# Kernel tuning notes

Measured on AMD Instinct MI355X. Metric: run time of the kernel, lower is better.

## Reference

```python
import jax, jax.numpy as jnp
import numpy as np
import math

NEG = -1000000.0

def setup_inputs() -> dict:
    key = jax.random.key(0)
    k1, k2, k3, k4 = jax.random.split(key, 4)
    B, S, D = 64, 1024, 64
    query = jax.random.normal(k1, (B, S, D), dtype=jnp.float32)
    key_t = jax.random.normal(k2, (B, S, D), dtype=jnp.float32)
    value = jax.random.normal(k3, (B, S, D), dtype=jnp.float32)
    valid_lens = jax.random.randint(k4, (B,), 1, S + 1, dtype=jnp.int32)
    return {"query": query, "key": key_t, "value": value, "valid_lens": valid_lens}

def reference(query, key, value, valid_lens):
    # query/key/value: [B, S, D]; valid_lens: [B]
    d = query.shape[-1]
    scores = jnp.einsum('bqd,bkd->bqk', query, key) / math.sqrt(d)
    Sk = key.shape[1]
    # 1D valid_lens -> same mask for every query row (repeat_interleave semantics)
    mask = jnp.arange(Sk)[None, None, :] < valid_lens[:, None, None]  # [B,1,Sk]
    scores = jnp.where(mask, scores, NEG)
    weights = jax.nn.softmax(scores, axis=-1)
    # dropout p=0.0 -> identity
    return jnp.einsum('bqk,bkd->bqd', weights, value)
```

## Files before the change

kernel.cpp:

```cpp
#include <hip/hip_runtime.h>
#include <hip/hip_bf16.h>
#include <cstdint>


typedef __attribute__((ext_vector_type(8))) short short8;
typedef __attribute__((ext_vector_type(4))) float f32x4;

#define B_   64
#define S_   1024
#define D_   64
#define BQ   64
#define BK   64
#define KPAD 72

__device__ __forceinline__ uint32_t pk2(float a, float b) {
    float2 t; t.x = a; t.y = b;
    union { __hip_bfloat162 h; uint32_t u; } c;
    c.h = __float22bfloat162_rn(t);
    return c.u;
}

__global__ __launch_bounds__(256, 4)
void attn_fwd(const float* __restrict__ Q, const float* __restrict__ K,
              const float* __restrict__ V, const int* __restrict__ VL,
              float* __restrict__ Out) {
    __shared__ __align__(16) unsigned short lK [BK * KPAD];
    __shared__ __align__(16) unsigned short lVt[D_ * 64];
    __shared__ __align__(16) unsigned short lP [4 * 16 * KPAD];

    const int tid  = threadIdx.x;
    const int wave = tid >> 6;
    const int lane = tid & 63;
    const int col  = lane & 15;
    const int quad = lane >> 4;

    const int bid  = blockIdx.x;
    const int b    = (bid & 7) * 8 + (bid >> 7);
    const int q0   = ((bid >> 3) & 15) * BQ;
    const int vlen = VL[b];
    const int ntiles = (vlen + BK - 1) / BK;

    const int T  = tid >> 4;
    const int m  = tid & 15;
    const int Tl = T & 3;
    const int cb = T >> 2;
    const int dcs = m >> 1;
    const int sws = ((dcs & 1) << 2) | (dcs >> 1);

    const float* Kb = K + (size_t)b * S_ * D_ + 4 * m;
    const float* Vb = V + (size_t)b * S_ * D_ + 4 * m;

    float4 kr[4], vr[4];
    #pragma unroll
    for (int j = 0; j < 4; ++j) {
        const int row = 2 * T + (j >> 1) * 32 + (j & 1);
        kr[j] = *(const float4*)(Kb + (size_t)row * D_);
        vr[j] = *(const float4*)(Vb + (size_t)row * D_);
    }

    short8 qa[2];
    {
        const int qrow = q0 + wave * 16 + col;
        const float* qp = Q + ((size_t)b * S_ + qrow) * D_ + quad * 8;
        #pragma unroll
        for (int c = 0; c < 2; ++c) {
            float4 x0 = *(const float4*)(qp + c * 32);
            float4 x1 = *(const float4*)(qp + c * 32 + 4);
            union { uint32_t u[4]; short8 s; } qq;
            qq.u[0] = pk2(x0.x, x0.y);
            qq.u[1] = pk2(x0.z, x0.w);
            qq.u[2] = pk2(x1.x, x1.y);
            qq.u[3] = pk2(x1.z, x1.w);
            qa[c] = qq.s;
        }
    }

    f32x4 ofrag[4];
    #pragma unroll
    for (int dt = 0; dt < 4; ++dt) ofrag[dt] = (f32x4){0.f, 0.f, 0.f, 0.f};
    float lsum = 0.f;

    const float cexp = 0.18033688011112042f;
    unsigned short* pw = &lP[wave * 16 * KPAD];

    for (int kt = 0; kt < ntiles; ++kt) {
        const int kbase = kt * BK;

        __syncthreads();

        #pragma unroll
        for (int j = 0; j < 4; ++j) {
            const int row = 2 * T + (j >> 1) * 32 + (j & 1);
            uint2 kv;
            kv.x = pk2(kr[j].x, kr[j].y);
            kv.y = pk2(kr[j].z, kr[j].w);
            *(uint2*)&lK[row * KPAD + 4 * m] = kv;
        }
        #pragma unroll
        for (int i = 0; i < 2; ++i) {
            const int p = (cb + 4 * i) ^ sws;
            unsigned short* base = &lVt[p * 8 + 2 * Tl];
            const float4 va = vr[2 * i], vb2 = vr[2 * i + 1];
            *(uint32_t*)&base[(4 * m + 0) * 64] = pk2(va.x, vb2.x);
            *(uint32_t*)&base[(4 * m + 1) * 64] = pk2(va.y, vb2.y);
            *(uint32_t*)&base[(4 * m + 2) * 64] = pk2(va.z, vb2.z);
            *(uint32_t*)&base[(4 * m + 3) * 64] = pk2(va.w, vb2.w);
        }

        if (kt + 1 < ntiles) {
            const size_t off = (size_t)(kt + 1) * BK * D_;
            #pragma unroll
            for (int j = 0; j < 4; ++j) {
                const int row = 2 * T + (j >> 1) * 32 + (j & 1);
                kr[j] = *(const float4*)(Kb + off + (size_t)row * D_);
                vr[j] = *(const float4*)(Vb + off + (size_t)row * D_);
            }
        }

        __syncthreads();

        f32x4 sfrag[4];
        #pragma unroll
        for (int ct = 0; ct < 4; ++ct) {
            f32x4 acc = (f32x4){0.f, 0.f, 0.f, 0.f};
            #pragma unroll
            for (int c = 0; c < 2; ++c) {
                short8 kf = *(const short8*)&lK[(ct * 16 + col) * KPAD + c * 32 + quad * 8];
                acc = __builtin_amdgcn_mfma_f32_16x16x32_bf16(kf, qa[c], acc, 0, 0, 0);
            }
            sfrag[ct] = acc;
        }

        if (kbase + BK <= vlen) {
            #pragma unroll
            for (int ct = 0; ct < 4; ++ct) {
                float e0 = __builtin_amdgcn_exp2f(sfrag[ct][0] * cexp);
                float e1 = __builtin_amdgcn_exp2f(sfrag[ct][1] * cexp);
                float e2 = __builtin_amdgcn_exp2f(sfrag[ct][2] * cexp);
                float e3 = __builtin_amdgcn_exp2f(sfrag[ct][3] * cexp);
                lsum += (e0 + e1) + (e2 + e3);
                uint2 pk; pk.x = pk2(e0, e1); pk.y = pk2(e2, e3);
                *(uint2*)&pw[col * KPAD + ct * 16 + quad * 4] = pk;
            }
        } else {
            #pragma unroll
            for (int ct = 0; ct < 4; ++ct) {
                const int kv0 = kbase + ct * 16 + quad * 4;
                float e[4];
                #pragma unroll
                for (int rr = 0; rr < 4; ++rr) {
                    e[rr] = (kv0 + rr < vlen)
                          ? __builtin_amdgcn_exp2f(sfrag[ct][rr] * cexp) : 0.0f;
                    lsum += e[rr];
                }
                uint2 pk; pk.x = pk2(e[0], e[1]); pk.y = pk2(e[2], e[3]);
                *(uint2*)&pw[col * KPAD + ct * 16 + quad * 4] = pk;
            }
        }

        #pragma unroll
        for (int kc = 0; kc < 2; ++kc) {
            short8 pa = *(const short8*)&pw[col * KPAD + kc * 32 + quad * 8];
            #pragma unroll
            for (int dt = 0; dt < 4; ++dt) {
                const int sr = ((col >> 3) << 2) | dt;
                const int p  = (kc * 4 + quad) ^ sr;
                short8 vb = *(const short8*)&lVt[(dt * 16 + col) * 64 + p * 8];
                ofrag[dt] = __builtin_amdgcn_mfma_f32_16x16x32_bf16(pa, vb, ofrag[dt], 0, 0, 0);
            }
        }
    }

    float s = lsum;
    s += __shfl_xor(s, 16, 64);
    s += __shfl_xor(s, 32, 64);
    const int qrow0 = q0 + wave * 16 + quad * 4;
    #pragma unroll
    for (int rr = 0; rr < 4; ++rr) {
        const float inv = 1.0f / __shfl(s, quad * 4 + rr, 64);
        float* op = Out + ((size_t)b * S_ + qrow0 + rr) * D_ + col;
        #pragma unroll
        for (int dt = 0; dt < 4; ++dt)
            op[dt * 16] = ofrag[dt][rr] * inv;
    }
}

extern "C" void kernel_launch(void* const* d_in, const int* in_sizes, int n_in,
                              void* d_out, int out_size, void* d_ws, size_t ws_size,
                              hipStream_t stream) {
    const float* Q  = (const float*)d_in[0];
    const float* K  = (const float*)d_in[1];
    const float* V  = (const float*)d_in[2];
    const int*   VL = (const int*)d_in[3];
    float* Out = (float*)d_out;
    dim3 grid(B_ * (S_ / BQ));
    attn_fwd<<<grid, 256, 0, stream>>>(Q, K, V, VL, Out);
}
```

Baseline: 115.0 us.

## Load K fragments directly from global per wave and double-buffer V in LDS

K is no longer staged through shared memory. Each wave loads its K MFMA fragments straight from global memory and converts them to bf16 in registers. V staging becomes double-buffered, which cuts the loop to one barrier per tile. This removes the K LDS writes and reads and one __syncthreads per iteration. In exchange, each of the four waves in a block now reads the whole K tile from global or L2 (4x redundant) with no prefetch, so load latency may be exposed. An unused pbf helper is also added.

After: 188.9 us. 1.64x slower.

```diff
diff --git a/kernel.cpp b/kernel.cpp
--- a/kernel.cpp
+++ b/kernel.cpp
@@ -11,7 +11,7 @@
 #define D_   64
 #define BQ   64
 #define BK   64
-#define KPAD 72
+#define PPAD 72
 
 __device__ __forceinline__ uint32_t pk2(float a, float b) {
     float2 t; t.x = a; t.y = b;
@@ -19,14 +19,17 @@
     c.h = __float22bfloat162_rn(t);
     return c.u;
 }
+__device__ __forceinline__ unsigned short pbf(float f) {
+    union { float f; uint32_t u; } v; v.f = f;
+    return (unsigned short)((v.u + 0x8000u) >> 16);
+}
 
 __global__ __launch_bounds__(256, 4)
 void attn_fwd(const float* __restrict__ Q, const float* __restrict__ K,
               const float* __restrict__ V, const int* __restrict__ VL,
               float* __restrict__ Out) {
-    __shared__ __align__(16) unsigned short lK [BK * KPAD];
-    __shared__ __align__(16) unsigned short lVt[D_ * 64];
-    __shared__ __align__(16) unsigned short lP [4 * 16 * KPAD];
+    __shared__ __align__(16) unsigned short lVt[2][D_ * 64];
+    __shared__ __align__(16) unsigned short lP [4 * 16 * PPAD];
 
     const int tid  = threadIdx.x;
     const int wave = tid >> 6;
@@ -47,14 +50,12 @@
     const int dcs = m >> 1;
     const int sws = ((dcs & 1) << 2) | (dcs >> 1);
 
-    const float* Kb = K + (size_t)b * S_ * D_ + 4 * m;
     const float* Vb = V + (size_t)b * S_ * D_ + 4 * m;
 
-    float4 kr[4], vr[4];
+    float4 vr[4];
     #pragma unroll
     for (int j = 0; j < 4; ++j) {
         const int row = 2 * T + (j >> 1) * 32 + (j & 1);
-        kr[j] = *(const float4*)(Kb + (size_t)row * D_);
         vr[j] = *(const float4*)(Vb + (size_t)row * D_);
     }
 
@@ -75,31 +76,24 @@
         }
     }
 
+    const float* Kw = K + ((size_t)b * S_ + col) * D_ + quad * 8;
+
     f32x4 ofrag[4];
     #pragma unroll
     for (int dt = 0; dt < 4; ++dt) ofrag[dt] = (f32x4){0.f, 0.f, 0.f, 0.f};
     float lsum = 0.f;
 
     const float cexp = 0.18033688011112042f;
-    unsigned short* pw = &lP[wave * 16 * KPAD];
+    unsigned short* pw = &lP[wave * 16 * PPAD];
 
     for (int kt = 0; kt < ntiles; ++kt) {
         const int kbase = kt * BK;
-
-        __syncthreads();
-
-        #pragma unroll
-        for (int j = 0; j < 4; ++j) {
-            const int row = 2 * T + (j >> 1) * 32 + (j & 1);
-            uint2 kv;
-            kv.x = pk2(kr[j].x, kr[j].y);
-            kv.y = pk2(kr[j].z, kr[j].w);
-            *(uint2*)&lK[row * KPAD + 4 * m] = kv;
-        }
+        unsigned short* bV = lVt[kt & 1];
+
         #pragma unroll
         for (int i = 0; i < 2; ++i) {
             const int p = (cb + 4 * i) ^ sws;
-            unsigned short* base = &lVt[p * 8 + 2 * Tl];
+            unsigned short* base = &bV[p * 8 + 2 * Tl];
             const float4 va = vr[2 * i], vb2 = vr[2 * i + 1];
             *(uint32_t*)&base[(4 * m + 0) * 64] = pk2(va.x, vb2.x);
             *(uint32_t*)&base[(4 * m + 1) * 64] = pk2(va.y, vb2.y);
@@ -107,40 +101,51 @@
             *(uint32_t*)&base[(4 * m + 3) * 64] = pk2(va.w, vb2.w);
         }
 
+        __syncthreads();
+
         if (kt + 1 < ntiles) {
-            const size_t off = (size_t)(kt + 1) * BK * D_;
+            const float* vp = Vb + (size_t)(kbase + BK) * D_;
             #pragma unroll
             for (int j = 0; j < 4; ++j) {
                 const int row = 2 * T + (j >> 1) * 32 + (j & 1);
-                kr[j] = *(const float4*)(Kb + off + (size_t)row * D_);
-                vr[j] = *(const float4*)(Vb + off + (size_t)row * D_);
-            }
-        }
-
-        __syncthreads();
-
-        f32x4 sfrag[4];
-        #pragma unroll
-        for (int ct = 0; ct < 4; ++ct) {
-            f32x4 acc = (f32x4){0.f, 0.f, 0.f, 0.f};
-            #pragma unroll
-            for (int c = 0; c < 2; ++c) {
-                short8 kf = *(const short8*)&lK[(ct * 16 + col) * KPAD + c * 32 + quad * 8];
-                acc = __builtin_amdgcn_mfma_f32_16x16x32_bf16(kf, qa[c], acc, 0, 0, 0);
-            }
-            sfrag[ct] = acc;
+                vr[j] = *(const float4*)(vp + (size_t)row * D_);
+            }
+        }
+
+        f32x4 sf[4];
+        #pragma unroll
+        for (int ct = 0; ct < 4; ++ct) sf[ct] = (f32x4){0.f, 0.f, 0.f, 0.f};
+        const float* Kt = Kw + (size_t)kbase * D_;
+        #pragma unroll
+        for (int c = 0; c < 2; ++c) {
+            short8 kf[4];
+            #pragma unroll
+            for (int ct = 0; ct < 4; ++ct) {
+                const float* kp = Kt + ct * 16 * D_ + c * 32;
+                float4 x0 = *(const float4*)kp;
+                float4 x1 = *(const float4*)(kp + 4);
+                union { uint32_t u[4]; short8 s; } kk;
+                kk.u[0] = pk2(x0.x, x0.y);
+                kk.u[1] = pk2(x0.z, x0.w);
+                kk.u[2] = pk2(x1.x, x1.y);
+                kk.u[3] = pk2(x1.z, x1.w);
+                kf[ct] = kk.s;
+            }
+            #pragma unroll
+            for (int ct = 0; ct < 4; ++ct)
+                sf[ct] = __builtin_amdgcn_mfma_f32_16x16x32_bf16(kf[ct], qa[c], sf[ct], 0, 0, 0);
         }
 
         if (kbase + BK <= vlen) {
             #pragma unroll
             for (int ct = 0; ct < 4; ++ct) {
-                float e0 = __builtin_amdgcn_exp2f(sfrag[ct][0] * cexp);
-                float e1 = __builtin_amdgcn_exp2f(sfrag[ct][1] * cexp);
-                float e2 = __builtin_amdgcn_exp2f(sfrag[ct][2] * cexp);
-                float e3 = __builtin_amdgcn_exp2f(sfrag[ct][3] * cexp);
+                float e0 = __builtin_amdgcn_exp2f(sf[ct][0] * cexp);
+                float e1 = __builtin_amdgcn_exp2f(sf[ct][1] * cexp);
+                float e2 = __builtin_amdgcn_exp2f(sf[ct][2] * cexp);
+                float e3 = __builtin_amdgcn_exp2f(sf[ct][3] * cexp);
                 lsum += (e0 + e1) + (e2 + e3);
                 uint2 pk; pk.x = pk2(e0, e1); pk.y = pk2(e2, e3);
-                *(uint2*)&pw[col * KPAD + ct * 16 + quad * 4] = pk;
+                *(uint2*)&pw[col * PPAD + ct * 16 + quad * 4] = pk;
             }
         } else {
             #pragma unroll
@@ -150,22 +155,22 @@
                 #pragma unroll
                 for (int rr = 0; rr < 4; ++rr) {
                     e[rr] = (kv0 + rr < vlen)
-                          ? __builtin_amdgcn_exp2f(sfrag[ct][rr] * cexp) : 0.0f;
+                          ? __builtin_amdgcn_exp2f(sf[ct][rr] * cexp) : 0.0f;
                     lsum += e[rr];
                 }
                 uint2 pk; pk.x = pk2(e[0], e[1]); pk.y = pk2(e[2], e[3]);
-                *(uint2*)&pw[col * KPAD + ct * 16 + quad * 4] = pk;
+                *(uint2*)&pw[col * PPAD + ct * 16 + quad * 4] = pk;
             }
         }
 
         #pragma unroll
         for (int kc = 0; kc < 2; ++kc) {
-            short8 pa = *(const short8*)&pw[col * KPAD + kc * 32 + quad * 8];
+            short8 pa = *(const short8*)&pw[col * PPAD + kc * 32 + quad * 8];
             #pragma unroll
             for (int dt = 0; dt < 4; ++dt) {
                 const int sr = ((col >> 3) << 2) | dt;
                 const int p  = (kc * 4 + quad) ^ sr;
-                short8 vb = *(const short8*)&lVt[(dt * 16 + col) * 64 + p * 8];
+                short8 vb = *(const short8*)&bV[(dt * 16 + col) * 64 + p * 8];
                 ofrag[dt] = __builtin_amdgcn_mfma_f32_16x16x32_bf16(pa, vb, ofrag[dt], 0, 0, 0);
             }
         }
```
